# Optimization experiments

Hardware: AMD Instinct MI355X
Metric: run time of the kernel (lower is better)

Reference implementation:

```python
import jax, jax.numpy as jnp
import numpy as np

NUM_QUERIES = 1024
NUM_DATASETS = 8
DB_SIZE = 32768
KEY_FEATURES = 64
VALUE_FEATURES = 64
NUM_NEIGHBORS = 128


def setup_inputs() -> dict:
    key = jax.random.key(0)
    k1, k2, k3 = jax.random.split(key, 3)
    query = jax.random.normal(k1, (NUM_QUERIES, NUM_DATASETS, KEY_FEATURES), dtype=jnp.float32)
    key_db = jax.random.normal(k2, (NUM_DATASETS, DB_SIZE, KEY_FEATURES), dtype=jnp.float32)
    value_db = jax.random.normal(k3, (NUM_DATASETS, DB_SIZE, VALUE_FEATURES), dtype=jnp.float32)
    return {"query": query, "key_db": key_db, "value_db": value_db, "num_neighbors": NUM_NEIGHBORS}


def reference(query, key_db, value_db, num_neighbors):
    # query: (Q, D, F); key_db: (D, DB, F); value_db: (D, DB, Fv)
    D, DB, F = key_db.shape
    Q = query.shape[0]
    Fv = value_db.shape[-1]
    num_buckets = num_neighbors
    bucket_size = DB // num_buckets

    q = jnp.moveaxis(query, 1, 0)                         # (D, Q, F)
    scores = jnp.einsum('dqf,dnf->dqn', q, key_db)        # (D, Q, DB)
    # mask out empty (all-zero) database slots
    mask = (key_db.sum(-1) == 0).astype(scores.dtype) * -1000000.0  # (D, DB)
    scores = scores + mask[:, None, :]

    # bucketize: DB = bucket_size * num_buckets, row-major reshape matches torch
    reshaped = scores.reshape(D, Q, bucket_size, num_buckets)
    # near-hard softmax over the bucket axis (soft-argmax trick)
    sparse = jax.nn.softmax(reshaped * 1000000.0, axis=2)  # (D, Q, bucket_size, num_buckets)

    key_r = key_db.reshape(D, bucket_size, num_buckets, F)
    val_r = value_db.reshape(D, bucket_size, num_buckets, Fv)
    sel_k = jnp.einsum('dqbn,dbnf->dqnf', sparse, key_r)   # (D, Q, N, F)
    sel_v = jnp.einsum('dqbn,dbnf->dqnf', sparse, val_r)   # (D, Q, N, Fv)

    selected_keys = jnp.moveaxis(sel_k, 0, 1)              # (Q, D, N, F)
    selected_values = jnp.moveaxis(sel_v, 0, 1)            # (Q, D, N, Fv)
    return selected_keys, selected_values
```

## Files before the change

kernel.cpp:

```cpp
#include <hip/hip_runtime.h>

#define D_   8
#define Q_   1024
#define DB_  32768
#define F_   64
#define NB_  128
#define BS_  256
#define NT_  (Q_*D_*NB_)
#define SPLIT_ 8
#define MARGIN_  5e-4f
#define MARGIN2_ 2e-4
#define FLAG_CAP_ 262144

typedef __attribute__((ext_vector_type(16))) float    f32x16;
typedef __attribute__((ext_vector_type(4)))  float    f32x4;
typedef __attribute__((ext_vector_type(8)))  short    short8;
typedef __attribute__((ext_vector_type(4)))  unsigned uint4v;
typedef __attribute__((ext_vector_type(8)))  __bf16   bf16x8;

static __device__ __forceinline__ f32x16 mfma32(short8 a, short8 b, f32x16 c) {
    return __builtin_amdgcn_mfma_f32_32x32x16_bf16(
        __builtin_bit_cast(bf16x8, a), __builtin_bit_cast(bf16x8, b), c, 0, 0, 0);
}

static __device__ __forceinline__ unsigned bfr(float x) {
    unsigned u = __float_as_uint(x);
    return (u + 0x7fffu + ((u >> 16) & 1u)) & 0xFFFF0000u;
}
static __device__ __forceinline__ unsigned cvt_hi(float x0, float x1) {
    return __builtin_amdgcn_perm(bfr(x1), bfr(x0), 0x07060302u);
}
static __device__ __forceinline__ unsigned cvt_lo(float x0, float x1) {
    unsigned a = bfr(x0), b = bfr(x1);
    unsigned la = bfr(x0 - __uint_as_float(a));
    unsigned lb = bfr(x1 - __uint_as_float(b));
    return __builtin_amdgcn_perm(lb, la, 0x07060302u);
}
static __device__ __forceinline__ void cvt8(float4 p, float4 q,
                                            uint4v& h, uint4v& l) {
    unsigned h0 = cvt_hi(p.x, p.y), l0 = cvt_lo(p.x, p.y);
    unsigned h1 = cvt_hi(p.z, p.w), l1 = cvt_lo(p.z, p.w);
    unsigned h2 = cvt_hi(q.x, q.y), l2 = cvt_lo(q.x, q.y);
    unsigned h3 = cvt_hi(q.z, q.w), l3 = cvt_lo(q.z, q.w);
    uint4v hh = { h0, h1, h2, h3 };
    uint4v ll = { l0, l1, l2, l3 };
    h = hh; l = ll;
}

__global__ __launch_bounds__(512, 4) void k_scan_mfma(
    const float* __restrict__ key_db, const float* __restrict__ query,
    float* __restrict__ m1p, float* __restrict__ m2p,
    unsigned char* __restrict__ b1p)
{
    __shared__ short kbuf[2][2][128][72];
    const int tid  = threadIdx.x;
    const int d    = blockIdx.x & 7;
    const int idx  = blockIdx.x >> 3;
    const int qi   = idx & 15;
    const int half = idx >> 4;
    const int q0 = qi * 64;
    const int wv = tid >> 6, lane = tid & 63;
    const int qg = wv >> 2, jg = wv & 3;
    const int lrow = lane & 31, kg = lane >> 5;

    short8 qh[4], ql[4];
    {
        const float* qr = query + ((size_t)(q0 + qg * 32 + lrow) * D_ + d) * F_ + kg * 8;
#pragma unroll
        for (int ks = 0; ks < 4; ++ks) {
            float4 A = *(const float4*)(qr + ks * 16);
            float4 B = *(const float4*)(qr + ks * 16 + 4);
            uint4v h, l;
            cvt8(A, B, h, l);
            qh[ks] = __builtin_bit_cast(short8, h);
            ql[ks] = __builtin_bit_cast(short8, l);
        }
    }

    float m1[16], m2[16]; int b1[16];
#pragma unroll
    for (int r = 0; r < 16; ++r) { m1[r] = -3e38f; m2[r] = -3e38f; b1[r] = 0; }

    const int nsteps = BS_ / SPLIT_;
    const int bstart = half * nsteps;
    const int r0 = tid >> 3, sub8 = (tid & 7) * 8;
    const float* sp = key_db + (size_t)d * DB_ * F_ + (size_t)bstart * NB_ * F_
                    + (size_t)r0 * F_ + sub8;

    {
        float4 A0 = *(const float4*)(sp);
        float4 A1 = *(const float4*)(sp + 4);
        float4 B0 = *(const float4*)(sp + 4096);
        float4 B1 = *(const float4*)(sp + 4096 + 4);
        uint4v h0, l0, h1, l1;
        cvt8(A0, A1, h0, l0);
        cvt8(B0, B1, h1, l1);
        *(short8*)&kbuf[0][0][r0     ][sub8] = __builtin_bit_cast(short8, h0);
        *(short8*)&kbuf[0][0][r0 + 64][sub8] = __builtin_bit_cast(short8, h1);
        *(short8*)&kbuf[0][1][r0     ][sub8] = __builtin_bit_cast(short8, l0);
        *(short8*)&kbuf[0][1][r0 + 64][sub8] = __builtin_bit_cast(short8, l1);
    }

    const int jrow = jg * 32 + lrow;
    int cur = 0;
    for (int p = 0; p < nsteps; ++p) {
        __syncthreads();
        float4 A0, A1, B0, B1;
        if (p + 1 < nsteps) {
            const float* np = sp + (size_t)(p + 1) * (NB_ * F_);
            A0 = *(const float4*)(np);
            A1 = *(const float4*)(np + 4);
            B0 = *(const float4*)(np + 4096);
            B1 = *(const float4*)(np + 4096 + 4);
        }

        f32x16 c = {0,0,0,0,0,0,0,0,0,0,0,0,0,0,0,0};
#pragma unroll
        for (int ks = 0; ks < 4; ++ks) {
            short8 kf = *(const short8*)&kbuf[cur][0][jrow][ks * 16 + kg * 8];
            c = mfma32(qh[ks], kf, c);
            c = mfma32(ql[ks], kf, c);
        }
#pragma unroll
        for (int ks = 0; ks < 4; ++ks) {
            short8 kf = *(const short8*)&kbuf[cur][1][jrow][ks * 16 + kg * 8];
            c = mfma32(qh[ks], kf, c);
        }

        const int b = bstart + p;
#pragma unroll
        for (int r = 0; r < 16; ++r) {
            float v = c[r];
            b1[r] = (v > m1[r]) ? b : b1[r];
            m2[r] = __builtin_amdgcn_fmed3f(v, m1[r], m2[r]);
            m1[r] = fmaxf(m1[r], v);
        }

        if (p + 1 < nsteps) {
            uint4v h0, l0, h1, l1;
            cvt8(A0, A1, h0, l0);
            cvt8(B0, B1, h1, l1);
            const int nb = cur ^ 1;
            *(short8*)&kbuf[nb][0][r0     ][sub8] = __builtin_bit_cast(short8, h0);
            *(short8*)&kbuf[nb][0][r0 + 64][sub8] = __builtin_bit_cast(short8, h1);
            *(short8*)&kbuf[nb][1][r0     ][sub8] = __builtin_bit_cast(short8, l0);
            *(short8*)&kbuf[nb][1][r0 + 64][sub8] = __builtin_bit_cast(short8, l1);
            cur = nb;
        }
    }

#pragma unroll
    for (int r = 0; r < 16; ++r) {
        const int q = q0 + qg * 32 + 4 * kg + (r & 3) + 8 * (r >> 2);
        const size_t t = (((size_t)q * D_ + d) << 7) + jrow;
        const size_t pp = (size_t)half * NT_ + t;
        m1p[pp] = m1[r]; m2p[pp] = m2[r]; b1p[pp] = (unsigned char)b1[r];
    }
}

__global__ void k_merge(const float* __restrict__ m1p, const float* __restrict__ m2p,
                        const unsigned char* __restrict__ b1p,
                        unsigned char* __restrict__ idx0b,
                        int* __restrict__ flag_cnt, int* __restrict__ flag_list)
{
    int t = blockIdx.x * 256 + threadIdx.x;
    if (t >= NT_) return;
    float m1 = -3e38f, m2 = -3e38f;
    int i1 = 0;
#pragma unroll
    for (int h = 0; h < SPLIT_; ++h) {
        float a    = m1p[(size_t)h * NT_ + t];
        float bsec = m2p[(size_t)h * NT_ + t];
        int   ib   = b1p[(size_t)h * NT_ + t];
        if (a > m1) { m2 = m1; m1 = a; i1 = ib; }
        else if (a > m2) m2 = a;
        if (bsec > m2) m2 = bsec;
    }
    idx0b[t] = (unsigned char)i1;
    if (m2 >= m1 - MARGIN_) {
        int pos = atomicAdd(flag_cnt, 1);
        if (pos < FLAG_CAP_) flag_list[pos] = t;
    }
}

__global__ void k_fixA(const float* __restrict__ query, const float* __restrict__ key_db,
                       const int* __restrict__ flag_cnt, const int* __restrict__ flag_list,
                       unsigned char* __restrict__ idx0b, int* __restrict__ flag2_cnt,
                       int* __restrict__ flag2_list)
{
    int cnt = *flag_cnt;
    if (cnt > FLAG_CAP_) cnt = FLAG_CAP_;
    int gw   = (blockIdx.x * blockDim.x + threadIdx.x) >> 6;
    int lane = threadIdx.x & 63;
    int nw   = (gridDim.x * blockDim.x) >> 6;

    for (int w = gw; w < cnt; w += nw) {
        int t = flag_list[w];
        int j = t & 127, d = (t >> 7) & 7, qi = t >> 10;
        const float* qrow = query + ((size_t)qi * D_ + d) * F_;
        const float* kb = key_db + (size_t)d * DB_ * F_;

        double m1 = -1e300, m2 = -1e300; int i1 = 0;
#pragma unroll
        for (int i = 0; i < 4; ++i) {
            int b = lane * 4 + i;
            const float* krow = kb + ((size_t)b * NB_ + j) * F_;
            double a = 0.0;
            for (int k2 = 0; k2 < F_; ++k2) a += (double)qrow[k2] * (double)krow[k2];
            if (a > m1) { m2 = m1; m1 = a; i1 = b; }
            else if (a > m2) m2 = a;
        }
        for (int off = 32; off; off >>= 1) {
            double om1 = __shfl_xor(m1, off);
            double om2 = __shfl_xor(m2, off);
            int    oi  = __shfl_xor(i1, off);
            if (om1 > m1) { m2 = fmax(m1, om2); m1 = om1; i1 = oi; }
            else          { m2 = fmax(m2, om1); }
        }
        if (lane == 0) {
            idx0b[t] = (unsigned char)i1;
            if (m1 - m2 < MARGIN2_) {
                int pos = atomicAdd(flag2_cnt, 1);
                if (pos < 4096) flag2_list[pos] = t;
            }
        }
    }
}

__global__ void k_gather(const float* __restrict__ key_db, const float* __restrict__ value_db,
                         const unsigned char* __restrict__ idx0b, f32x4* __restrict__ out)
{
    const int total = NT_ * 16 * 2;
    for (int e = blockIdx.x * 256 + threadIdx.x; e < total; e += gridDim.x * 256) {
        int half = e >> 24;
        int rem  = e & 0xFFFFFF;
        int t  = rem >> 4;
        int fc = rem & 15;
        int j = t & 127;
        int d = (t >> 7) & 7;
        int b = idx0b[t];
        const float* db = half ? value_db : key_db;
        int n = b * NB_ + j;
        f32x4 v = *reinterpret_cast<const f32x4*>(db + ((size_t)d * DB_ + n) * F_ + fc * 4);
        __builtin_nontemporal_store(v, &out[e]);
    }
}

__global__ void k_fixB(const float* __restrict__ query, const float* __restrict__ key_db,
                       const float* __restrict__ value_db, const int* __restrict__ flag_cnt,
                       const int* __restrict__ flag_list, float* __restrict__ out)
{
    int cnt = *flag_cnt;
    if (cnt > 4096) cnt = 4096;
    int gw   = (blockIdx.x * blockDim.x + threadIdx.x) >> 6;
    int lane = threadIdx.x & 63;
    int nw   = (gridDim.x * blockDim.x) >> 6;

    for (int w = gw; w < cnt; w += nw) {
        int t = flag_list[w];
        int j = t & 127, d = (t >> 7) & 7, qi = t >> 10;
        const float* qrow = query + ((size_t)qi * D_ + d) * F_;
        const float* kb = key_db + (size_t)d * DB_ * F_;
        const float* vb = value_db + (size_t)d * DB_ * F_;

        double sv[4];
#pragma unroll
        for (int i = 0; i < 4; ++i) {
            int b = lane * 4 + i;
            const float* krow = kb + ((size_t)b * NB_ + j) * F_;
            double a = 0.0;
            for (int k2 = 0; k2 < F_; ++k2) a += (double)qrow[k2] * (double)krow[k2];
            sv[i] = a;
        }
        double m = fmax(fmax(sv[0], sv[1]), fmax(sv[2], sv[3]));
        for (int off = 32; off; off >>= 1) m = fmax(m, __shfl_xor(m, off));
        double ev[4];
        double es = 0.0;
#pragma unroll
        for (int i = 0; i < 4; ++i) { ev[i] = exp((sv[i] - m) * 1e6); es += ev[i]; }
        for (int off = 32; off; off >>= 1) es += __shfl_xor(es, off);
        double inv = 1.0 / es;
#pragma unroll
        for (int i = 0; i < 4; ++i) ev[i] *= inv;

        double ak = 0.0, av = 0.0;
        for (int src = 0; src < 64; ++src) {
#pragma unroll
            for (int i = 0; i < 4; ++i) {
                double wv = __shfl(ev[i], src);
                if (wv > 1e-300) {
                    int b = src * 4 + i;
                    size_t o = ((size_t)b * NB_ + j) * F_ + lane;
                    ak += wv * (double)kb[o];
                    av += wv * (double)vb[o];
                }
            }
        }
        out[(size_t)t * F_ + lane] = (float)ak;
        out[(size_t)NT_ * F_ + (size_t)t * F_ + lane] = (float)av;
    }
}

extern "C" void kernel_launch(void* const* d_in, const int* in_sizes, int n_in,
                              void* d_out, int out_size, void* d_ws, size_t ws_size,
                              hipStream_t stream)
{
    const float* query    = (const float*)d_in[0];
    const float* key_db   = (const float*)d_in[1];
    const float* value_db = (const float*)d_in[2];
    float* out = (float*)d_out;

    unsigned char* idx0b = (unsigned char*)d_ws;
    int* flag_cnt   = (int*)((char*)d_ws + (size_t)NT_);
    int* flag2_cnt  = flag_cnt + 1;
    int* flag_list  = (int*)((char*)d_ws + (size_t)NT_ + 256);
    int* flag2_list = flag_list + FLAG_CAP_;

    float* m1p = (float*)d_out;
    float* m2p = m1p + (size_t)SPLIT_ * NT_;
    unsigned char* b1p = (unsigned char*)(m2p + (size_t)SPLIT_ * NT_);

    (void)hipMemsetAsync(flag_cnt, 0, 8, stream);

    k_scan_mfma<<<1024, 512, 0, stream>>>(key_db, query, m1p, m2p, b1p);
    k_merge    <<<NT_ / 256, 256, 0, stream>>>(m1p, m2p, b1p, idx0b, flag_cnt, flag_list);
    k_fixA     <<<512,  256, 0, stream>>>(query, key_db, flag_cnt, flag_list,
                                          idx0b, flag2_cnt, flag2_list);
    k_gather   <<<2048, 256, 0, stream>>>(key_db, value_db, idx0b, (f32x4*)d_out);
    k_fixB     <<<256,  256, 0, stream>>>(query, key_db, value_db, flag2_cnt,
                                          flag2_list, out);
}
```

Before: 339.5 us.

## Load keys directly into registers and pack bucket index into score low bits

The scan kernel drops the double-buffered LDS staging of bf16-split keys. Each wave now loads its key rows straight from global memory and converts them to hi/lo bf16 in registers, with only a periodic barrier. The argmax bucket index is packed into the low 8 mantissa bits of the score, which removes the separate b1 array and its byte partial buffer in the merge. The conversion uses native bf16 casts, and the merge margin is widened to make up for the precision lost to index packing. In exchange, keys are loaded redundantly per wave, and more entries may be flagged for the fix-up kernels.

```diff
diff --git a/kernel.cpp b/kernel.cpp
--- a/kernel.cpp
+++ b/kernel.cpp
@@ -8,14 +8,13 @@
 #define BS_  256
 #define NT_  (Q_*D_*NB_)
 #define SPLIT_ 8
-#define MARGIN_  5e-4f
+#define MARGIN_  6e-4f
 #define MARGIN2_ 2e-4
 #define FLAG_CAP_ 262144
 
 typedef __attribute__((ext_vector_type(16))) float    f32x16;
 typedef __attribute__((ext_vector_type(4)))  float    f32x4;
 typedef __attribute__((ext_vector_type(8)))  short    short8;
-typedef __attribute__((ext_vector_type(4)))  unsigned uint4v;
 typedef __attribute__((ext_vector_type(8)))  __bf16   bf16x8;
 
 static __device__ __forceinline__ f32x16 mfma32(short8 a, short8 b, f32x16 c) {
@@ -23,36 +22,27 @@
         __builtin_bit_cast(bf16x8, a), __builtin_bit_cast(bf16x8, b), c, 0, 0, 0);
 }
 
-static __device__ __forceinline__ unsigned bfr(float x) {
-    unsigned u = __float_as_uint(x);
-    return (u + 0x7fffu + ((u >> 16) & 1u)) & 0xFFFF0000u;
-}
-static __device__ __forceinline__ unsigned cvt_hi(float x0, float x1) {
-    return __builtin_amdgcn_perm(bfr(x1), bfr(x0), 0x07060302u);
-}
-static __device__ __forceinline__ unsigned cvt_lo(float x0, float x1) {
-    unsigned a = bfr(x0), b = bfr(x1);
-    unsigned la = bfr(x0 - __uint_as_float(a));
-    unsigned lb = bfr(x1 - __uint_as_float(b));
-    return __builtin_amdgcn_perm(lb, la, 0x07060302u);
-}
-static __device__ __forceinline__ void cvt8(float4 p, float4 q,
-                                            uint4v& h, uint4v& l) {
-    unsigned h0 = cvt_hi(p.x, p.y), l0 = cvt_lo(p.x, p.y);
-    unsigned h1 = cvt_hi(p.z, p.w), l1 = cvt_lo(p.z, p.w);
-    unsigned h2 = cvt_hi(q.x, q.y), l2 = cvt_lo(q.x, q.y);
-    unsigned h3 = cvt_hi(q.z, q.w), l3 = cvt_lo(q.z, q.w);
-    uint4v hh = { h0, h1, h2, h3 };
-    uint4v ll = { l0, l1, l2, l3 };
-    h = hh; l = ll;
+static __device__ __forceinline__ void cvt8f(float4 a, float4 b,
+                                             short8& kh, short8& kl) {
+    float x0 = a.x, x1 = a.y, x2 = a.z, x3 = a.w;
+    float x4 = b.x, x5 = b.y, x6 = b.z, x7 = b.w;
+    bf16x8 h, l;
+    h[0] = (__bf16)x0; l[0] = (__bf16)(x0 - (float)h[0]);
+    h[1] = (__bf16)x1; l[1] = (__bf16)(x1 - (float)h[1]);
+    h[2] = (__bf16)x2; l[2] = (__bf16)(x2 - (float)h[2]);
+    h[3] = (__bf16)x3; l[3] = (__bf16)(x3 - (float)h[3]);
+    h[4] = (__bf16)x4; l[4] = (__bf16)(x4 - (float)h[4]);
+    h[5] = (__bf16)x5; l[5] = (__bf16)(x5 - (float)h[5]);
+    h[6] = (__bf16)x6; l[6] = (__bf16)(x6 - (float)h[6]);
+    h[7] = (__bf16)x7; l[7] = (__bf16)(x7 - (float)h[7]);
+    kh = __builtin_bit_cast(short8, h);
+    kl = __builtin_bit_cast(short8, l);
 }
 
 __global__ __launch_bounds__(512, 4) void k_scan_mfma(
     const float* __restrict__ key_db, const float* __restrict__ query,
-    float* __restrict__ m1p, float* __restrict__ m2p,
-    unsigned char* __restrict__ b1p)
-{
-    __shared__ short kbuf[2][2][128][72];
+    float* __restrict__ m1p, float* __restrict__ m2p)
+{
     const int tid  = threadIdx.x;
     const int d    = blockIdx.x & 7;
     const int idx  = blockIdx.x >> 3;
@@ -70,83 +60,44 @@
         for (int ks = 0; ks < 4; ++ks) {
             float4 A = *(const float4*)(qr + ks * 16);
             float4 B = *(const float4*)(qr + ks * 16 + 4);
-            uint4v h, l;
-            cvt8(A, B, h, l);
-            qh[ks] = __builtin_bit_cast(short8, h);
-            ql[ks] = __builtin_bit_cast(short8, l);
-        }
-    }
-
-    float m1[16], m2[16]; int b1[16];
-#pragma unroll
-    for (int r = 0; r < 16; ++r) { m1[r] = -3e38f; m2[r] = -3e38f; b1[r] = 0; }
+            cvt8f(A, B, qh[ks], ql[ks]);
+        }
+    }
+
+    float m1q[16], m2[16];
+#pragma unroll
+    for (int r = 0; r < 16; ++r) { m1q[r] = -3e38f; m2[r] = -3e38f; }
 
     const int nsteps = BS_ / SPLIT_;
     const int bstart = half * nsteps;
-    const int r0 = tid >> 3, sub8 = (tid & 7) * 8;
-    const float* sp = key_db + (size_t)d * DB_ * F_ + (size_t)bstart * NB_ * F_
-                    + (size_t)r0 * F_ + sub8;
-
-    {
-        float4 A0 = *(const float4*)(sp);
-        float4 A1 = *(const float4*)(sp + 4);
-        float4 B0 = *(const float4*)(sp + 4096);
-        float4 B1 = *(const float4*)(sp + 4096 + 4);
-        uint4v h0, l0, h1, l1;
-        cvt8(A0, A1, h0, l0);
-        cvt8(B0, B1, h1, l1);
-        *(short8*)&kbuf[0][0][r0     ][sub8] = __builtin_bit_cast(short8, h0);
-        *(short8*)&kbuf[0][0][r0 + 64][sub8] = __builtin_bit_cast(short8, h1);
-        *(short8*)&kbuf[0][1][r0     ][sub8] = __builtin_bit_cast(short8, l0);
-        *(short8*)&kbuf[0][1][r0 + 64][sub8] = __builtin_bit_cast(short8, l1);
-    }
-
     const int jrow = jg * 32 + lrow;
-    int cur = 0;
+    const size_t kstep = (size_t)NB_ * F_;
+    const float* kp = key_db + (size_t)d * DB_ * F_
+                    + ((size_t)bstart * NB_ + jrow) * F_ + kg * 8;
+
     for (int p = 0; p < nsteps; ++p) {
-        __syncthreads();
-        float4 A0, A1, B0, B1;
-        if (p + 1 < nsteps) {
-            const float* np = sp + (size_t)(p + 1) * (NB_ * F_);
-            A0 = *(const float4*)(np);
-            A1 = *(const float4*)(np + 4);
-            B0 = *(const float4*)(np + 4096);
-            B1 = *(const float4*)(np + 4096 + 4);
-        }
-
         f32x16 c = {0,0,0,0,0,0,0,0,0,0,0,0,0,0,0,0};
 #pragma unroll
         for (int ks = 0; ks < 4; ++ks) {
-            short8 kf = *(const short8*)&kbuf[cur][0][jrow][ks * 16 + kg * 8];
-            c = mfma32(qh[ks], kf, c);
-            c = mfma32(ql[ks], kf, c);
-        }
-#pragma unroll
-        for (int ks = 0; ks < 4; ++ks) {
-            short8 kf = *(const short8*)&kbuf[cur][1][jrow][ks * 16 + kg * 8];
-            c = mfma32(qh[ks], kf, c);
-        }
-
-        const int b = bstart + p;
+            float4 A = *(const float4*)(kp + ks * 16);
+            float4 B = *(const float4*)(kp + ks * 16 + 4);
+            short8 kh, kl;
+            cvt8f(A, B, kh, kl);
+            c = mfma32(qh[ks], kh, c);
+            c = mfma32(ql[ks], kh, c);
+            c = mfma32(qh[ks], kl, c);
+        }
+        kp += kstep;
+
+        const unsigned bb = (unsigned)(bstart + p);
 #pragma unroll
         for (int r = 0; r < 16; ++r) {
-            float v = c[r];
-            b1[r] = (v > m1[r]) ? b : b1[r];
-            m2[r] = __builtin_amdgcn_fmed3f(v, m1[r], m2[r]);
-            m1[r] = fmaxf(m1[r], v);
-        }
-
-        if (p + 1 < nsteps) {
-            uint4v h0, l0, h1, l1;
-            cvt8(A0, A1, h0, l0);
-            cvt8(B0, B1, h1, l1);
-            const int nb = cur ^ 1;
-            *(short8*)&kbuf[nb][0][r0     ][sub8] = __builtin_bit_cast(short8, h0);
-            *(short8*)&kbuf[nb][0][r0 + 64][sub8] = __builtin_bit_cast(short8, h1);
-            *(short8*)&kbuf[nb][1][r0     ][sub8] = __builtin_bit_cast(short8, l0);
-            *(short8*)&kbuf[nb][1][r0 + 64][sub8] = __builtin_bit_cast(short8, l1);
-            cur = nb;
-        }
+            float vq = __uint_as_float((__float_as_uint(c[r]) & 0xFFFFFF00u) | bb);
+            m2[r]  = __builtin_amdgcn_fmed3f(vq, m1q[r], m2[r]);
+            m1q[r] = (vq > m1q[r]) ? vq : m1q[r];
+        }
+
+        if ((p & 7) == 7) __syncthreads();
     }
 
 #pragma unroll
@@ -154,29 +105,26 @@
         const int q = q0 + qg * 32 + 4 * kg + (r & 3) + 8 * (r >> 2);
         const size_t t = (((size_t)q * D_ + d) << 7) + jrow;
         const size_t pp = (size_t)half * NT_ + t;
-        m1p[pp] = m1[r]; m2p[pp] = m2[r]; b1p[pp] = (unsigned char)b1[r];
+        m1p[pp] = m1q[r]; m2p[pp] = m2[r];
     }
 }
 
 __global__ void k_merge(const float* __restrict__ m1p, const float* __restrict__ m2p,
-                        const unsigned char* __restrict__ b1p,
                         unsigned char* __restrict__ idx0b,
                         int* __restrict__ flag_cnt, int* __restrict__ flag_list)
 {
     int t = blockIdx.x * 256 + threadIdx.x;
     if (t >= NT_) return;
     float m1 = -3e38f, m2 = -3e38f;
-    int i1 = 0;
 #pragma unroll
     for (int h = 0; h < SPLIT_; ++h) {
         float a    = m1p[(size_t)h * NT_ + t];
         float bsec = m2p[(size_t)h * NT_ + t];
-        int   ib   = b1p[(size_t)h * NT_ + t];
-        if (a > m1) { m2 = m1; m1 = a; i1 = ib; }
+        if (a > m1) { m2 = m1; m1 = a; }
         else if (a > m2) m2 = a;
         if (bsec > m2) m2 = bsec;
     }
-    idx0b[t] = (unsigned char)i1;
+    idx0b[t] = (unsigned char)(__float_as_uint(m1) & 0xFFu);
     if (m2 >= m1 - MARGIN_) {
         int pos = atomicAdd(flag_cnt, 1);
         if (pos < FLAG_CAP_) flag_list[pos] = t;
@@ -318,12 +266,11 @@
 
     float* m1p = (float*)d_out;
     float* m2p = m1p + (size_t)SPLIT_ * NT_;
-    unsigned char* b1p = (unsigned char*)(m2p + (size_t)SPLIT_ * NT_);
 
     (void)hipMemsetAsync(flag_cnt, 0, 8, stream);
 
-    k_scan_mfma<<<1024, 512, 0, stream>>>(key_db, query, m1p, m2p, b1p);
-    k_merge    <<<NT_ / 256, 256, 0, stream>>>(m1p, m2p, b1p, idx0b, flag_cnt, flag_list);
+    k_scan_mfma<<<1024, 512, 0, stream>>>(key_db, query, m1p, m2p);
+    k_merge    <<<NT_ / 256, 256, 0, stream>>>(m1p, m2p, idx0b, flag_cnt, flag_list);
     k_fixA     <<<512,  256, 0, stream>>>(query, key_db, flag_cnt, flag_list,
                                           idx0b, flag2_cnt, flag2_list);
     k_gather   <<<2048, 256, 0, stream>>>(key_db, value_db, idx0b, (f32x4*)d_out);
```

New measurement: 424.8 us. 25.1% more time.
